# Performance work log

Hardware: AMD Instinct MI355X
Metric: run time of the kernel (lower is better)

The kernel has to match this reference:

```python
import jax, jax.numpy as jnp
import numpy as np

B, C, H, W = 8, 2048, 14, 14
NUM_CLASSES, WORD_DIM, INTER_DIM = 80, 300, 1024


def setup_inputs() -> dict:
    key = jax.random.key(0)
    ks = jax.random.split(key, 8)
    s = 0.02
    return {
        "image_features": jax.random.normal(ks[0], (B, C, H, W), jnp.float32),
        "word_features": jax.random.normal(ks[1], (NUM_CLASSES, WORD_DIM), jnp.float32),
        "W1": jax.random.normal(ks[2], (INTER_DIM, C), jnp.float32) * s,
        "W2": jax.random.normal(ks[3], (INTER_DIM, WORD_DIM), jnp.float32) * s,
        "W3": jax.random.normal(ks[4], (INTER_DIM, INTER_DIM), jnp.float32) * s,
        "b3": jax.random.normal(ks[5], (INTER_DIM,), jnp.float32) * s,
        "Wa": jax.random.normal(ks[6], (1, INTER_DIM), jnp.float32) * s,
        "ba": jax.random.normal(ks[7], (1,), jnp.float32) * s,
        "num_classes": NUM_CLASSES,
    }


def reference(image_features, word_features, W1, W2, W3, b3, Wa, ba, num_classes):
    b, c, h, w = image_features.shape
    # [s, b, c] with s = h*w (spatial locations)
    img = image_features.reshape(b, c, h * w).transpose(2, 0, 1)
    f_wh = img @ W1.T                      # [s, b, D]
    f_wd = word_features @ W2.T            # [n, D]
    # additive-attention score MLP; broadcast to [s, b, n, D]
    lb = jnp.tanh(f_wh[:, :, None, :] * f_wd[None, None, :, :]) @ W3.T + b3
    coef = (lb @ Wa.T + ba)[..., 0]        # [s, b, n]
    coef = jax.nn.softmax(coef, axis=0)    # softmax over spatial locations
    # weighted sum over spatial dim -> [b, n, c]
    return jnp.einsum('sbc,sbn->bnc', img, coef)
```

## Files before the change

kernel.cpp:

```cpp
#include <hip/hip_runtime.h>
#include <math.h>

#define SB 196
#define SP 224
#define NB 8
#define NC 2048
#define ND 1024
#define NN 80
#define NW 300
#define CH 32
#define DCH (ND / CH)
#define NT 4
#define NJ (NB * SB)
#define NJP 1600
#define PITCH 40

typedef __bf16 v8bf __attribute__((ext_vector_type(8)));
typedef __bf16 v4bf __attribute__((ext_vector_type(4)));
typedef float  f32x4 __attribute__((ext_vector_type(4)));

__global__ __launch_bounds__(256) void kcast_x(const float* __restrict__ X,
                                               const float* __restrict__ W1,
                                               const float* __restrict__ W2,
                                               const float* __restrict__ W3,
                                               const float* __restrict__ Wa,
                                               __bf16* __restrict__ Xt,
                                               __bf16* __restrict__ Xhi,
                                               __bf16* __restrict__ Xlo,
                                               __bf16* __restrict__ W1b,
                                               float* __restrict__ vpart,
                                               float* __restrict__ W2t) {
    const int t = threadIdx.x;
    if (blockIdx.z == 10) {
        if (blockIdx.x >= 20) return;
        __shared__ float tw[64][65];
        int id = blockIdx.y * 20 + blockIdx.x;
        int dt = id / 5, wt = id - dt * 5;
        int d0 = dt * 64, w0 = wt * 64;
        {
            int ss = t & 63, cbase = t >> 6;
            #pragma unroll
            for (int r = 0; r < 16; ++r) {
                int cc = cbase + 4 * r;
                tw[cc][ss] = (w0 + ss < NW) ? W2[(size_t)(d0 + cc) * NW + w0 + ss] : 0.f;
            }
        }
        __syncthreads();
        {
            int cc = t & 63, sbase = t >> 6;
            #pragma unroll
            for (int r = 0; r < 16; ++r) {
                int ss = sbase + 4 * r;
                if (w0 + ss < NW)
                    W2t[(size_t)(w0 + ss) * ND + d0 + cc] = tw[cc][ss];
            }
        }
        return;
    }
    if (blockIdx.z == 9) {
        if (blockIdx.x < 16) {
            const int e0 = blockIdx.x * 64;
            const int d  = blockIdx.y * 256 + t;
            float p = 0.f;
            #pragma unroll 8
            for (int e = e0; e < e0 + 64; ++e)
                p += Wa[e] * W3[(size_t)e * ND + d];
            vpart[blockIdx.x * ND + d] = p;
        } else if (blockIdx.x == 16) {
            const int tid = blockIdx.y * 256 + t;
            uint4 z = make_uint4(0u, 0u, 0u, 0u);
            uint4* p = (uint4*)(Xt + (size_t)NJ * NC);
            #pragma unroll
            for (int r = 0; r < 8; ++r) p[tid + r * 1024] = z;
        }
        return;
    }
    if (blockIdx.z == 8) {
        unsigned int slice_tid = (blockIdx.x * 4 + blockIdx.y) * 256 + t;
        #pragma unroll 4
        for (int r = 0; r < 16; ++r) {
            size_t i = ((size_t)slice_tid + (size_t)r * 32768) * 4;
            float4 f = *(const float4*)(W1 + i);
            v4bf o;
            o[0] = (__bf16)f.x; o[1] = (__bf16)f.y;
            o[2] = (__bf16)f.z; o[3] = (__bf16)f.w;
            *(v4bf*)(W1b + i) = o;
        }
        return;
    }
    __shared__ float tile[64][65];
    const int b  = blockIdx.z;
    const int c0 = blockIdx.x * 64;
    const int s0 = blockIdx.y * 64;
    const float* Xb = X + (size_t)b * NC * SB;
    {
        int ss = t & 63, cbase = t >> 6;
        #pragma unroll
        for (int r = 0; r < 16; ++r) {
            int cc = cbase + 4 * r;
            float val = (s0 + ss < SB) ? Xb[(size_t)(c0 + cc) * SB + s0 + ss] : 0.f;
            tile[cc][ss] = val;
        }
    }
    __syncthreads();
    {
        int cc = t & 63, sbase = t >> 6;
        #pragma unroll
        for (int r = 0; r < 16; ++r) {
            int ss = sbase + 4 * r;
            if (s0 + ss < SB)
                Xt[((size_t)b * SB + s0 + ss) * NC + c0 + cc] = (__bf16)tile[cc][ss];
        }
    }
    {
        int ss = t & 63, cbase = t >> 6;
        int sg = s0 + ss;
        #pragma unroll
        for (int r = 0; r < 16; ++r) {
            int cc = cbase + 4 * r;
            if (sg < SP) {
                float val = (sg < SB) ? tile[cc][ss] : 0.f;
                __bf16 h = (__bf16)val;
                __bf16 l = (__bf16)(val - (float)h);
                size_t base = ((size_t)b * NC + c0 + cc) * SP + sg;
                Xhi[base] = h;
                Xlo[base] = l;
            }
        }
    }
}

__global__ __launch_bounds__(256) void k1_mfma(const __bf16* __restrict__ Xt,
                                               const __bf16* __restrict__ W1b,
                                               float* __restrict__ F,
                                               const float* __restrict__ word,
                                               const float* __restrict__ W2t,
                                               const float* __restrict__ vpart,
                                               float2* __restrict__ wpack) {
    const int t = threadIdx.x;
    if (blockIdx.y >= 25) {
        __shared__ __align__(16) float lword[NW];
        const int e = (blockIdx.y - 25) * 16 + blockIdx.x;
        const int n = e >> 2;
        const int d = (e & 3) * 256 + t;
        for (int i = t; i < NW; i += 256) lword[i] = word[(size_t)n * NW + i];
        __syncthreads();
        float acc = 0.f;
        #pragma unroll 10
        for (int w = 0; w < NW; ++w)
            acc = fmaf(lword[w], W2t[(size_t)w * ND + d], acc);
        float vv = 0.f;
        #pragma unroll
        for (int p = 0; p < 16; ++p) vv += vpart[p * ND + d];
        float2 o;
        o.x = 2.8853900817779268f * acc;
        o.y = -2.f * vv;
        wpack[(size_t)n * ND + d] = o;
        return;
    }
    __shared__ __align__(16) __bf16 lA[64 * PITCH];
    __shared__ __align__(16) __bf16 lB[64 * PITCH];
    const int d0   = blockIdx.x * 64;
    const int j0   = blockIdx.y * 64;
    const int lane = t & 63;
    const int wave = t >> 6;
    const int doff = (wave & 1) * 32;
    const int joff = (wave >> 1) * 32;
    const int quad = lane >> 4;
    const int l16  = lane & 15;

    f32x4 acc[2][2] = {};

    const int rr = t >> 2;
    const int cc = (t & 3) * 8;
    const __bf16* Ag = W1b + (size_t)(d0 + rr) * NC + cc;
    const __bf16* Bg = Xt + (size_t)(j0 + rr) * NC + cc;
    __bf16* lAw = lA + rr * PITCH + cc;
    __bf16* lBw = lB + rr * PITCH + cc;

    const __bf16* rA0 = lA + (doff + l16) * PITCH + quad * 8;
    const __bf16* rA1 = rA0 + 16 * PITCH;
    const __bf16* rB0 = lB + (joff + l16) * PITCH + quad * 8;
    const __bf16* rB1 = rB0 + 16 * PITCH;

    for (int k0 = 0; k0 < NC; k0 += 32) {
        uint4 a  = *(const uint4*)(Ag + k0);
        uint4 bv = *(const uint4*)(Bg + k0);
        __syncthreads();
        *(uint4*)lAw = a;
        *(uint4*)lBw = bv;
        __syncthreads();
        v8bf a0 = *(const v8bf*)rA0;
        v8bf a1 = *(const v8bf*)rA1;
        v8bf b0 = *(const v8bf*)rB0;
        v8bf b1 = *(const v8bf*)rB1;
        acc[0][0] = __builtin_amdgcn_mfma_f32_16x16x32_bf16(a0, b0, acc[0][0], 0, 0, 0);
        acc[0][1] = __builtin_amdgcn_mfma_f32_16x16x32_bf16(a0, b1, acc[0][1], 0, 0, 0);
        acc[1][0] = __builtin_amdgcn_mfma_f32_16x16x32_bf16(a1, b0, acc[1][0], 0, 0, 0);
        acc[1][1] = __builtin_amdgcn_mfma_f32_16x16x32_bf16(a1, b1, acc[1][1], 0, 0, 0);
    }
    #pragma unroll
    for (int i = 0; i < 2; ++i) {
        #pragma unroll
        for (int jj = 0; jj < 2; ++jj) {
            int j = j0 + joff + jj * 16 + l16;
            if (j < NJ) {
                int b = j / SB;
                int s = j - b * SB;
                float* Fp = F + ((size_t)b * ND + d0 + doff + i * 16 + quad * 4) * SB + s;
                #pragma unroll
                for (int r = 0; r < 4; ++r)
                    Fp[(size_t)r * SB] = acc[i][jj][r];
            }
        }
    }
}

__global__ __launch_bounds__(256) void k2a(const float* __restrict__ F,
                                           const float2* __restrict__ wpack,
                                           float* __restrict__ part) {
    const int n0  = blockIdx.x * NT;
    const int ch  = blockIdx.z;
    const int idx = blockIdx.y * 256 + threadIdx.x;
    const bool valid = idx < (NB * SB);
    const int iv = valid ? idx : 0;
    const int b  = iv / SB;
    const int s  = iv - b * SB;
    const float*  Fp  = F + ((size_t)b * ND + ch * DCH) * SB + s;
    const float4* wp0 = (const float4*)(wpack + (size_t)(n0 + 0) * ND + ch * DCH);
    const float4* wp1 = (const float4*)(wpack + (size_t)(n0 + 1) * ND + ch * DCH);
    const float4* wp2 = (const float4*)(wpack + (size_t)(n0 + 2) * ND + ch * DCH);
    const float4* wp3 = (const float4*)(wpack + (size_t)(n0 + 3) * ND + ch * DCH);
    float a0 = 0.f, a1 = 0.f, a2 = 0.f, a3 = 0.f;
    #pragma unroll 4
    for (int d2 = 0; d2 < DCH / 2; ++d2) {
        float f0 = Fp[(size_t)(2 * d2)     * SB];
        float f1 = Fp[(size_t)(2 * d2 + 1) * SB];
        float4 w0 = wp0[d2];
        float4 w1 = wp1[d2];
        float4 w2 = wp2[d2];
        float4 w3 = wp3[d2];
        float e00 = __builtin_amdgcn_exp2f(f0 * w0.x);
        float e01 = __builtin_amdgcn_exp2f(f1 * w0.z);
        float e10 = __builtin_amdgcn_exp2f(f0 * w1.x);
        float e11 = __builtin_amdgcn_exp2f(f1 * w1.z);
        float e20 = __builtin_amdgcn_exp2f(f0 * w2.x);
        float e21 = __builtin_amdgcn_exp2f(f1 * w2.z);
        float e30 = __builtin_amdgcn_exp2f(f0 * w3.x);
        float e31 = __builtin_amdgcn_exp2f(f1 * w3.z);
        a0 = fmaf(w0.y, __builtin_amdgcn_rcpf(1.f + e00), a0);
        a0 = fmaf(w0.w, __builtin_amdgcn_rcpf(1.f + e01), a0);
        a1 = fmaf(w1.y, __builtin_amdgcn_rcpf(1.f + e10), a1);
        a1 = fmaf(w1.w, __builtin_amdgcn_rcpf(1.f + e11), a1);
        a2 = fmaf(w2.y, __builtin_amdgcn_rcpf(1.f + e20), a2);
        a2 = fmaf(w2.w, __builtin_amdgcn_rcpf(1.f + e21), a2);
        a3 = fmaf(w3.y, __builtin_amdgcn_rcpf(1.f + e30), a3);
        a3 = fmaf(w3.w, __builtin_amdgcn_rcpf(1.f + e31), a3);
    }
    if (valid) {
        size_t base = ((size_t)ch * NB + b) * NN;
        part[(base + n0 + 0) * 256 + s] = a0;
        part[(base + n0 + 1) * 256 + s] = a1;
        part[(base + n0 + 2) * 256 + s] = a2;
        part[(base + n0 + 3) * 256 + s] = a3;
    }
}

__global__ __launch_bounds__(256) void k2b(const float* __restrict__ part,
                                           __bf16* __restrict__ coefh,
                                           __bf16* __restrict__ coefl) {
    __shared__ float red[256];
    const int n = blockIdx.x;
    const int b = blockIdx.y;
    const int t = threadIdx.x;
    float acc = 0.f;
    #pragma unroll
    for (int ch = 0; ch < CH; ++ch)
        acc += part[(((size_t)ch * NB + b) * NN + n) * 256 + t];

    red[t] = (t < SB) ? acc : -1e30f;
    __syncthreads();
    #pragma unroll
    for (int off = 128; off > 0; off >>= 1) {
        if (t < off) red[t] = fmaxf(red[t], red[t + off]);
        __syncthreads();
    }
    float m = red[0];
    __syncthreads();
    float p = (t < SB) ? __expf(acc - m) : 0.f;
    red[t] = p;
    __syncthreads();
    #pragma unroll
    for (int off = 128; off > 0; off >>= 1) {
        if (t < off) red[t] += red[t + off];
        __syncthreads();
    }
    float inv = 1.f / red[0];
    if (t < SP) {
        float val = (t < SB) ? p * inv : 0.f;
        __bf16 h = (__bf16)val;
        __bf16 l = (__bf16)(val - (float)h);
        size_t base = ((size_t)b * NN + n) * SP + t;
        coefh[base] = h;
        coefl[base] = l;
    }
}

__global__ __launch_bounds__(256) void k3_mfma(const __bf16* __restrict__ Xhi,
                                               const __bf16* __restrict__ Xlo,
                                               const __bf16* __restrict__ coefh,
                                               const __bf16* __restrict__ coefl,
                                               float* __restrict__ out) {
    const int t     = threadIdx.x;
    const int wave  = t >> 6;
    const int lane  = t & 63;
    const int quad  = lane >> 4;
    const int l16   = lane & 15;
    const int b     = blockIdx.y;
    const int cbase = blockIdx.x * 64 + wave * 16;

    const __bf16* Bh = Xhi + ((size_t)b * NC + cbase + l16) * SP + quad * 8;
    const __bf16* Bl = Xlo + ((size_t)b * NC + cbase + l16) * SP + quad * 8;
    const __bf16* Ah = coefh + ((size_t)b * NN + l16) * SP + quad * 8;
    const __bf16* Al = coefl + ((size_t)b * NN + l16) * SP + quad * 8;

    f32x4 acc[5] = {};

    #pragma unroll
    for (int k0 = 0; k0 < SP; k0 += 32) {
        v8bf bh = *(const v8bf*)(Bh + k0);
        v8bf bl = *(const v8bf*)(Bl + k0);
        #pragma unroll
        for (int mt = 0; mt < 5; ++mt) {
            v8bf ah = *(const v8bf*)(Ah + (size_t)mt * 16 * SP + k0);
            v8bf al = *(const v8bf*)(Al + (size_t)mt * 16 * SP + k0);
            acc[mt] = __builtin_amdgcn_mfma_f32_16x16x32_bf16(ah, bh, acc[mt], 0, 0, 0);
            acc[mt] = __builtin_amdgcn_mfma_f32_16x16x32_bf16(al, bh, acc[mt], 0, 0, 0);
            acc[mt] = __builtin_amdgcn_mfma_f32_16x16x32_bf16(ah, bl, acc[mt], 0, 0, 0);
        }
    }
    #pragma unroll
    for (int mt = 0; mt < 5; ++mt) {
        #pragma unroll
        for (int r = 0; r < 4; ++r) {
            int n = mt * 16 + quad * 4 + r;
            out[((size_t)b * NN + n) * NC + cbase + l16] = acc[mt][r];
        }
    }
}

extern "C" void kernel_launch(void* const* d_in, const int* in_sizes, int n_in,
                              void* d_out, int out_size, void* d_ws, size_t ws_size,
                              hipStream_t stream) {
    const float* X    = (const float*)d_in[0];
    const float* word = (const float*)d_in[1];
    const float* W1   = (const float*)d_in[2];
    const float* W2   = (const float*)d_in[3];
    const float* W3   = (const float*)d_in[4];
    const float* Wa   = (const float*)d_in[6];
    float* out = (float*)d_out;

    char* ws = (char*)d_ws;
    float*  vpart = (float*)ws;
    float*  W2t   = vpart + 16 * ND;
    float2* wpack = (float2*)(W2t + (size_t)NW * ND);
    float*  part  = (float*)(wpack + (size_t)NN * ND);
    __bf16* coefh = (__bf16*)(part + (size_t)CH * NB * NN * 256);
    __bf16* coefl = coefh + (size_t)NB * NN * SP;
    __bf16* W1b   = coefl + (size_t)NB * NN * SP;
    __bf16* Xt    = W1b + (size_t)ND * NC;
    float*  F     = (float*)(Xt + (size_t)NJP * NC);
    __bf16* Xhi   = (__bf16*)(F + (size_t)NB * ND * SB);
    __bf16* Xlo   = Xhi + (size_t)NB * NC * SP;

    kcast_x<<<dim3(32, 4, 11),    256, 0, stream>>>(X, W1, W2, W3, Wa, Xt, Xhi, Xlo, W1b, vpart, W2t);
    k1_mfma<<<dim3(16, 45),       256, 0, stream>>>(Xt, W1b, F, word, W2t, vpart, wpack);
    k2a    <<<dim3(NN / NT, 7, CH), 256, 0, stream>>>(F, wpack, part);
    k2b    <<<dim3(NN, NB),       256, 0, stream>>>(part, coefh, coefl);
    k3_mfma<<<dim3(NC / 64, NB),  256, 0, stream>>>(Xhi, Xlo, coefh, coefl, out);
}
```

Baseline: 170.0 us.

## Fuse attention-score tanh reduction into GEMM epilogue and reshuffle prep kernels

The f_wh GEMM kernel no longer writes F to global memory. Its 64x64 output tile is staged in shared memory, and each wave computes the tanh-MLP partial scores for 20 classes over that tile's 64 d values, writing per-chunk partials (now 16 chunks instead of 32). The separate k2a kernel and the F round-trip through global memory are removed. The word-projection (wpack) work moves from the GEMM grid into the cast kernel, and the vpart/W2 transpose/zero-fill work moves to a new small prep kernel. The trade-off is that the GEMM blocks now carry a long serial epilogue (20 classes x 64 d per wave, each with exp and rcp) on only 400 blocks, which may lower occupancy and latency hiding compared with the wide standalone k2a grid.

Result: slower. 194.4 us (+14.4%).

```diff
diff --git a/kernel.cpp b/kernel.cpp
--- a/kernel.cpp
+++ b/kernel.cpp
@@ -8,9 +8,7 @@
 #define ND 1024
 #define NN 80
 #define NW 300
-#define CH 32
-#define DCH (ND / CH)
-#define NT 4
+#define CH 16
 #define NJ (NB * SB)
 #define NJP 1600
 #define PITCH 40
@@ -19,22 +17,25 @@
 typedef __bf16 v4bf __attribute__((ext_vector_type(4)));
 typedef float  f32x4 __attribute__((ext_vector_type(4)));
 
-__global__ __launch_bounds__(256) void kcast_x(const float* __restrict__ X,
-                                               const float* __restrict__ W1,
-                                               const float* __restrict__ W2,
-                                               const float* __restrict__ W3,
-                                               const float* __restrict__ Wa,
-                                               __bf16* __restrict__ Xt,
-                                               __bf16* __restrict__ Xhi,
-                                               __bf16* __restrict__ Xlo,
-                                               __bf16* __restrict__ W1b,
-                                               float* __restrict__ vpart,
-                                               float* __restrict__ W2t) {
+__global__ __launch_bounds__(256) void kprep(const float* __restrict__ W2,
+                                             const float* __restrict__ W3,
+                                             const float* __restrict__ Wa,
+                                             float* __restrict__ vpart,
+                                             float* __restrict__ W2t,
+                                             __bf16* __restrict__ Xt) {
     const int t = threadIdx.x;
-    if (blockIdx.z == 10) {
-        if (blockIdx.x >= 20) return;
+    const int bid = blockIdx.x;
+    if (bid < 64) {
+        const int e0 = (bid >> 2) * 64;
+        const int d  = (bid & 3) * 256 + t;
+        float p = 0.f;
+        #pragma unroll 8
+        for (int e = e0; e < e0 + 64; ++e)
+            p += Wa[e] * W3[(size_t)e * ND + d];
+        vpart[(bid >> 2) * ND + d] = p;
+    } else if (bid < 144) {
         __shared__ float tw[64][65];
-        int id = blockIdx.y * 20 + blockIdx.x;
+        int id = bid - 64;
         int dt = id / 5, wt = id - dt * 5;
         int d0 = dt * 64, w0 = wt * 64;
         {
@@ -55,24 +56,45 @@
                     W2t[(size_t)(w0 + ss) * ND + d0 + cc] = tw[cc][ss];
             }
         }
-        return;
-    }
-    if (blockIdx.z == 9) {
-        if (blockIdx.x < 16) {
-            const int e0 = blockIdx.x * 64;
-            const int d  = blockIdx.y * 256 + t;
-            float p = 0.f;
-            #pragma unroll 8
-            for (int e = e0; e < e0 + 64; ++e)
-                p += Wa[e] * W3[(size_t)e * ND + d];
-            vpart[blockIdx.x * ND + d] = p;
-        } else if (blockIdx.x == 16) {
-            const int tid = blockIdx.y * 256 + t;
-            uint4 z = make_uint4(0u, 0u, 0u, 0u);
-            uint4* p = (uint4*)(Xt + (size_t)NJ * NC);
-            #pragma unroll
-            for (int r = 0; r < 8; ++r) p[tid + r * 1024] = z;
-        }
+    } else {
+        const int tid = (bid - 144) * 256 + t;
+        uint4 z = make_uint4(0u, 0u, 0u, 0u);
+        uint4* p = (uint4*)(Xt + (size_t)NJ * NC);
+        #pragma unroll
+        for (int r = 0; r < 8; ++r) p[tid + r * 1024] = z;
+    }
+}
+
+__global__ __launch_bounds__(256) void kcast_x(const float* __restrict__ X,
+                                               const float* __restrict__ W1,
+                                               const float* __restrict__ word,
+                                               const float* __restrict__ vpart,
+                                               const float* __restrict__ W2t,
+                                               __bf16* __restrict__ Xt,
+                                               __bf16* __restrict__ Xhi,
+                                               __bf16* __restrict__ Xlo,
+                                               __bf16* __restrict__ W1b,
+                                               float2* __restrict__ wpack) {
+    const int t = threadIdx.x;
+    if (blockIdx.z >= 9) {
+        const int e = (blockIdx.z - 9) * 128 + blockIdx.x * 4 + blockIdx.y;
+        if (e >= 320) return;
+        __shared__ __align__(16) float lword[NW];
+        const int n = e >> 2;
+        const int d = (e & 3) * 256 + t;
+        for (int i = t; i < NW; i += 256) lword[i] = word[(size_t)n * NW + i];
+        __syncthreads();
+        float acc = 0.f;
+        #pragma unroll 10
+        for (int w = 0; w < NW; ++w)
+            acc = fmaf(lword[w], W2t[(size_t)w * ND + d], acc);
+        float vv = 0.f;
+        #pragma unroll
+        for (int p = 0; p < 16; ++p) vv += vpart[p * ND + d];
+        float2 o;
+        o.x = 2.8853900817779268f * acc;
+        o.y = -2.f * vv;
+        wpack[(size_t)n * ND + d] = o;
         return;
     }
     if (blockIdx.z == 8) {
@@ -132,34 +154,14 @@
 
 __global__ __launch_bounds__(256) void k1_mfma(const __bf16* __restrict__ Xt,
                                                const __bf16* __restrict__ W1b,
-                                               float* __restrict__ F,
-                                               const float* __restrict__ word,
-                                               const float* __restrict__ W2t,
-                                               const float* __restrict__ vpart,
-                                               float2* __restrict__ wpack) {
-    const int t = threadIdx.x;
-    if (blockIdx.y >= 25) {
-        __shared__ __align__(16) float lword[NW];
-        const int e = (blockIdx.y - 25) * 16 + blockIdx.x;
-        const int n = e >> 2;
-        const int d = (e & 3) * 256 + t;
-        for (int i = t; i < NW; i += 256) lword[i] = word[(size_t)n * NW + i];
-        __syncthreads();
-        float acc = 0.f;
-        #pragma unroll 10
-        for (int w = 0; w < NW; ++w)
-            acc = fmaf(lword[w], W2t[(size_t)w * ND + d], acc);
-        float vv = 0.f;
-        #pragma unroll
-        for (int p = 0; p < 16; ++p) vv += vpart[p * ND + d];
-        float2 o;
-        o.x = 2.8853900817779268f * acc;
-        o.y = -2.f * vv;
-        wpack[(size_t)n * ND + d] = o;
-        return;
-    }
-    __shared__ __align__(16) __bf16 lA[64 * PITCH];
-    __shared__ __align__(16) __bf16 lB[64 * PITCH];
+                                               const float2* __restrict__ wpack,
+                                               float* __restrict__ part) {
+    __shared__ __align__(16) char smem[64 * 65 * 4];
+    __bf16* lA    = (__bf16*)smem;
+    __bf16* lB    = lA + 64 * PITCH;
+    float*  Ftile = (float*)smem;
+
+    const int t    = threadIdx.x;
     const int d0   = blockIdx.x * 64;
     const int j0   = blockIdx.y * 64;
     const int lane = t & 63;
@@ -199,70 +201,39 @@
         acc[1][0] = __builtin_amdgcn_mfma_f32_16x16x32_bf16(a1, b0, acc[1][0], 0, 0, 0);
         acc[1][1] = __builtin_amdgcn_mfma_f32_16x16x32_bf16(a1, b1, acc[1][1], 0, 0, 0);
     }
+
+    __syncthreads();
     #pragma unroll
     for (int i = 0; i < 2; ++i) {
         #pragma unroll
         for (int jj = 0; jj < 2; ++jj) {
-            int j = j0 + joff + jj * 16 + l16;
-            if (j < NJ) {
-                int b = j / SB;
-                int s = j - b * SB;
-                float* Fp = F + ((size_t)b * ND + d0 + doff + i * 16 + quad * 4) * SB + s;
-                #pragma unroll
-                for (int r = 0; r < 4; ++r)
-                    Fp[(size_t)r * SB] = acc[i][jj][r];
+            #pragma unroll
+            for (int r = 0; r < 4; ++r) {
+                Ftile[(doff + i * 16 + quad * 4 + r) * 65 + (joff + jj * 16 + l16)]
+                    = acc[i][jj][r];
             }
         }
     }
-}
-
-__global__ __launch_bounds__(256) void k2a(const float* __restrict__ F,
-                                           const float2* __restrict__ wpack,
-                                           float* __restrict__ part) {
-    const int n0  = blockIdx.x * NT;
-    const int ch  = blockIdx.z;
-    const int idx = blockIdx.y * 256 + threadIdx.x;
-    const bool valid = idx < (NB * SB);
-    const int iv = valid ? idx : 0;
-    const int b  = iv / SB;
-    const int s  = iv - b * SB;
-    const float*  Fp  = F + ((size_t)b * ND + ch * DCH) * SB + s;
-    const float4* wp0 = (const float4*)(wpack + (size_t)(n0 + 0) * ND + ch * DCH);
-    const float4* wp1 = (const float4*)(wpack + (size_t)(n0 + 1) * ND + ch * DCH);
-    const float4* wp2 = (const float4*)(wpack + (size_t)(n0 + 2) * ND + ch * DCH);
-    const float4* wp3 = (const float4*)(wpack + (size_t)(n0 + 3) * ND + ch * DCH);
-    float a0 = 0.f, a1 = 0.f, a2 = 0.f, a3 = 0.f;
-    #pragma unroll 4
-    for (int d2 = 0; d2 < DCH / 2; ++d2) {
-        float f0 = Fp[(size_t)(2 * d2)     * SB];
-        float f1 = Fp[(size_t)(2 * d2 + 1) * SB];
-        float4 w0 = wp0[d2];
-        float4 w1 = wp1[d2];
-        float4 w2 = wp2[d2];
-        float4 w3 = wp3[d2];
-        float e00 = __builtin_amdgcn_exp2f(f0 * w0.x);
-        float e01 = __builtin_amdgcn_exp2f(f1 * w0.z);
-        float e10 = __builtin_amdgcn_exp2f(f0 * w1.x);
-        float e11 = __builtin_amdgcn_exp2f(f1 * w1.z);
-        float e20 = __builtin_amdgcn_exp2f(f0 * w2.x);
-        float e21 = __builtin_amdgcn_exp2f(f1 * w2.z);
-        float e30 = __builtin_amdgcn_exp2f(f0 * w3.x);
-        float e31 = __builtin_amdgcn_exp2f(f1 * w3.z);
-        a0 = fmaf(w0.y, __builtin_amdgcn_rcpf(1.f + e00), a0);
-        a0 = fmaf(w0.w, __builtin_amdgcn_rcpf(1.f + e01), a0);
-        a1 = fmaf(w1.y, __builtin_amdgcn_rcpf(1.f + e10), a1);
-        a1 = fmaf(w1.w, __builtin_amdgcn_rcpf(1.f + e11), a1);
-        a2 = fmaf(w2.y, __builtin_amdgcn_rcpf(1.f + e20), a2);
-        a2 = fmaf(w2.w, __builtin_amdgcn_rcpf(1.f + e21), a2);
-        a3 = fmaf(w3.y, __builtin_amdgcn_rcpf(1.f + e30), a3);
-        a3 = fmaf(w3.w, __builtin_amdgcn_rcpf(1.f + e31), a3);
-    }
-    if (valid) {
-        size_t base = ((size_t)ch * NB + b) * NN;
-        part[(base + n0 + 0) * 256 + s] = a0;
-        part[(base + n0 + 1) * 256 + s] = a1;
-        part[(base + n0 + 2) * 256 + s] = a2;
-        part[(base + n0 + 3) * 256 + s] = a3;
+    __syncthreads();
+
+    const int wid   = __builtin_amdgcn_readfirstlane(wave);
+    const int jglob = j0 + lane;
+    const bool valid = jglob < NJ;
+    const int bi = jglob / SB;
+    const int s  = jglob - bi * SB;
+    const int ch = blockIdx.x;
+    for (int nn = 0; nn < 20; ++nn) {
+        const int n = wid * 20 + nn;
+        const float2* wrow = wpack + (size_t)n * ND + d0;
+        float p = 0.f;
+        #pragma unroll 8
+        for (int dd = 0; dd < 64; ++dd) {
+            float2 w  = wrow[dd];
+            float  Fv = Ftile[dd * 65 + lane];
+            p = fmaf(w.y, __builtin_amdgcn_rcpf(1.f + __builtin_amdgcn_exp2f(Fv * w.x)), p);
+        }
+        if (valid)
+            part[(((size_t)ch * NB + bi) * NN + n) * 256 + s] = p;
     }
 }
 
@@ -369,13 +340,12 @@
     __bf16* coefl = coefh + (size_t)NB * NN * SP;
     __bf16* W1b   = coefl + (size_t)NB * NN * SP;
     __bf16* Xt    = W1b + (size_t)ND * NC;
-    float*  F     = (float*)(Xt + (size_t)NJP * NC);
-    __bf16* Xhi   = (__bf16*)(F + (size_t)NB * ND * SB);
+    __bf16* Xhi   = Xt + (size_t)NJP * NC;
     __bf16* Xlo   = Xhi + (size_t)NB * NC * SP;
 
-    kcast_x<<<dim3(32, 4, 11),    256, 0, stream>>>(X, W1, W2, W3, Wa, Xt, Xhi, Xlo, W1b, vpart, W2t);
-    k1_mfma<<<dim3(16, 45),       256, 0, stream>>>(Xt, W1b, F, word, W2t, vpart, wpack);
-    k2a    <<<dim3(NN / NT, 7, CH), 256, 0, stream>>>(F, wpack, part);
-    k2b    <<<dim3(NN, NB),       256, 0, stream>>>(part, coefh, coefl);
-    k3_mfma<<<dim3(NC / 64, NB),  256, 0, stream>>>(Xhi, Xlo, coefh, coefl, out);
-}
+    kprep  <<<148,               256, 0, stream>>>(W2, W3, Wa, vpart, W2t, Xt);
+    kcast_x<<<dim3(32, 4, 12),   256, 0, stream>>>(X, W1, word, vpart, W2t, Xt, Xhi, Xlo, W1b, wpack);
+    k1_mfma<<<dim3(16, 25),      256, 0, stream>>>(Xt, W1b, wpack, part);
+    k2b    <<<dim3(NN, NB),      256, 0, stream>>>(part, coefh, coefl);
+    k3_mfma<<<dim3(NC / 64, NB), 256, 0, stream>>>(Xhi, Xlo, coefh, coefl, out);
+}
```
